# Optimization experiments

Hardware: AMD Instinct MI355X
Metric: run time of the kernel (lower is better)

## Reference

```python
import jax, jax.numpy as jnp
import numpy as np

N_NODES = 50000
N_EDGES = 800000
NODE_DIM = 128
IN_CH = 64
OUT_CH = 16
N_GRAPHS = 512
N_LAYERS = 5
BN_EPS = 1e-5


def setup_inputs() -> dict:
    key = jax.random.key(0)
    ks = jax.random.split(key, 16)
    s = lambda fan_in: 1.0 / np.sqrt(fan_in)
    inp = {
        "x": jax.random.normal(ks[0], (N_NODES, NODE_DIM), dtype=jnp.float32),
        "edge_index": jax.random.randint(ks[1], (2, N_EDGES), 0, N_NODES, dtype=jnp.int64),
        "batch": jnp.sort(jax.random.randint(ks[2], (N_NODES,), 0, N_GRAPHS, dtype=jnp.int64)),
        "enc_W": jax.random.normal(ks[3], (NODE_DIM, IN_CH), dtype=jnp.float32) * s(NODE_DIM),
        "enc_b": jnp.zeros((IN_CH,), dtype=jnp.float32),
        "conv_W1": jax.random.normal(ks[4], (N_LAYERS, IN_CH, IN_CH), dtype=jnp.float32) * s(IN_CH),
        "conv_b1": jnp.zeros((N_LAYERS, IN_CH), dtype=jnp.float32),
        "conv_W2": jax.random.normal(ks[5], (N_LAYERS, IN_CH, IN_CH), dtype=jnp.float32) * s(IN_CH),
        "conv_b2": jnp.zeros((N_LAYERS, IN_CH), dtype=jnp.float32),
        "bn_gamma": jnp.ones((N_LAYERS, IN_CH), dtype=jnp.float32),
        "bn_beta": jnp.zeros((N_LAYERS, IN_CH), dtype=jnp.float32),
        "fc1_W": jax.random.normal(ks[6], (IN_CH, IN_CH), dtype=jnp.float32) * s(IN_CH),
        "fc1_b": jnp.zeros((IN_CH,), dtype=jnp.float32),
        "fc2_W": jax.random.normal(ks[7], (IN_CH, OUT_CH), dtype=jnp.float32) * s(IN_CH),
        "fc2_b": jnp.zeros((OUT_CH,), dtype=jnp.float32),
    }
    return inp


def reference(x, edge_index, batch, enc_W, enc_b, conv_W1, conv_b1, conv_W2,
              conv_b2, bn_gamma, bn_beta, fc1_W, fc1_b, fc2_W, fc2_b):
    src, dst = edge_index[0], edge_index[1]
    # node feature encoder
    h = x @ enc_W + enc_b  # [N, C]
    for l in range(N_LAYERS):
        # GINConv (eps=0): (1+eps)*x + sum_{j->i} x_j, then 2-layer MLP
        agg = jax.ops.segment_sum(h[src], dst, num_segments=N_NODES)
        z = h + agg
        z = jax.nn.relu(z @ conv_W1[l] + conv_b1[l]) @ conv_W2[l] + conv_b2[l]
        z = jax.nn.relu(z)
        # BatchNorm1d (training stats, biased variance)
        mean = jnp.mean(z, axis=0)
        var = jnp.mean(jnp.square(z - mean), axis=0)
        h = (z - mean) * jax.lax.rsqrt(var + BN_EPS) * bn_gamma[l] + bn_beta[l]
    # global add pool over graphs
    g = jax.ops.segment_sum(h, batch, num_segments=N_GRAPHS)  # [G, C]
    g = jax.nn.relu(g @ fc1_W + fc1_b)
    # dropout is identity in eval mode
    out = g @ fc2_W + fc2_b  # [G, OUT_CH]
    return out
```

## Files before the change

kernel.cpp:

```cpp
#include <hip/hip_runtime.h>
#include <hip/hip_fp16.h>

#define N_NODES 50000
#define N_EDGES 800000
#define NODE_DIM 128
#define C 64
#define N_GRAPHS 512
#define N_LAYERS 5
#define BN_EPS 1e-5f

#define SCAN_BLOCKS 196
#define NBUCK 196
#define ECHUNK 4096

typedef unsigned int u32;
typedef unsigned short u16;

__device__ inline float2 h2f(u32 v) {
    __half2 h; __builtin_memcpy(&h, &v, 4);
    return __half22float2(h);
}
__device__ inline u32 f2h2(float a, float b) {
    __half2 h = __floats2half2_rn(a, b);
    u32 v; __builtin_memcpy(&v, &h, 4);
    return v;
}

__global__ __launch_bounds__(256) void enc_kernel(const float* __restrict__ x,
                                                  const float* __restrict__ W,
                                                  const float* __restrict__ b,
                                                  u32* __restrict__ z) {
    __shared__ float As[64 * 132];
    __shared__ float Ws[NODE_DIM * C];
    int t = threadIdx.x;
    int tc = t & 15, tr = t >> 4;
    for (int i = t; i < NODE_DIM * C; i += 256) Ws[i] = W[i];
    int row0 = blockIdx.x * 128;
    float4 bv = ((const float4*)b)[tc];
    float acc[8][4];
#pragma unroll
    for (int i = 0; i < 8; ++i) { acc[i][0] = bv.x; acc[i][1] = bv.y; acc[i][2] = bv.z; acc[i][3] = bv.w; }

    for (int kc = 0; kc < 2; ++kc) {
        __syncthreads();
        for (int it = 0; it < 8; ++it) {
            int idx = t + 256 * it;
            int r = idx >> 4, f4 = idx & 15;
            int grow = row0 + r;
            float4 v = (grow < N_NODES) ? ((const float4*)x)[grow * 32 + kc * 16 + f4]
                                        : make_float4(0.f, 0.f, 0.f, 0.f);
            int k4 = f4 * 4;
            As[(k4 + 0) * 132 + r] = v.x;
            As[(k4 + 1) * 132 + r] = v.y;
            As[(k4 + 2) * 132 + r] = v.z;
            As[(k4 + 3) * 132 + r] = v.w;
        }
        __syncthreads();
#pragma unroll 4
        for (int k = 0; k < 64; ++k) {
            const float* ap = As + k * 132 + tr * 8;
            float4 a0 = *(const float4*)(ap);
            float4 a1 = *(const float4*)(ap + 4);
            float4 w = *(const float4*)(Ws + (kc * 64 + k) * C + tc * 4);
            float av[8] = {a0.x, a0.y, a0.z, a0.w, a1.x, a1.y, a1.z, a1.w};
#pragma unroll
            for (int i = 0; i < 8; ++i) {
                acc[i][0] = fmaf(av[i], w.x, acc[i][0]);
                acc[i][1] = fmaf(av[i], w.y, acc[i][1]);
                acc[i][2] = fmaf(av[i], w.z, acc[i][2]);
                acc[i][3] = fmaf(av[i], w.w, acc[i][3]);
            }
        }
    }
#pragma unroll
    for (int i = 0; i < 8; ++i) {
        int grow = row0 + tr * 8 + i;
        if (grow < N_NODES) {
            uint2 o;
            o.x = f2h2(acc[i][0], acc[i][1]);
            o.y = f2h2(acc[i][2], acc[i][3]);
            ((uint2*)z)[grow * 16 + tc] = o;
        }
    }
}

__global__ __launch_bounds__(256) void csr_hist(const int* __restrict__ ei,
                                                int* __restrict__ bcount) {
    __shared__ int lhist[NBUCK];
    int t = threadIdx.x;
    if (t < NBUCK) lhist[t] = 0;
    __syncthreads();
    int e0 = blockIdx.x * ECHUNK;
    int e1 = min(e0 + ECHUNK, N_EDGES);
    for (int e = e0 + t; e < e1; e += 256)
        atomicAdd(&lhist[ei[N_EDGES + e] >> 8], 1);
    __syncthreads();
    if (t < NBUCK && lhist[t] > 0) atomicAdd(&bcount[t], lhist[t]);
}

__global__ __launch_bounds__(256) void csr_bscan(const int* __restrict__ bcount,
                                                 int* __restrict__ bbase,
                                                 int* __restrict__ bcursor,
                                                 int* __restrict__ offs) {
    __shared__ int s[256];
    int t = threadIdx.x;
    int v = (t < NBUCK) ? bcount[t] : 0;
    s[t] = v;
    for (int off = 1; off < 256; off <<= 1) {
        __syncthreads();
        int x = (t >= off) ? s[t - off] : 0;
        __syncthreads();
        s[t] += x;
    }
    __syncthreads();
    if (t < NBUCK) {
        bbase[t + 1] = s[t];
        bcursor[t] = s[t] - v;
    }
    if (t == 0) { bbase[0] = 0; offs[N_NODES] = N_EDGES; }
}

__global__ __launch_bounds__(256) void csr_stage(const int* __restrict__ ei,
                                                 int* __restrict__ bcursor,
                                                 u32* __restrict__ staged) {
    __shared__ int lhist[NBUCK];
    __shared__ int lbase[NBUCK];
    __shared__ int lcur[NBUCK];
    int t = threadIdx.x;
    if (t < NBUCK) lhist[t] = 0;
    __syncthreads();
    int e0 = blockIdx.x * ECHUNK;
    int e1 = min(e0 + ECHUNK, N_EDGES);
    for (int e = e0 + t; e < e1; e += 256)
        atomicAdd(&lhist[ei[N_EDGES + e] >> 8], 1);
    __syncthreads();
    if (t < NBUCK) {
        int c = lhist[t];
        lbase[t] = (c > 0) ? atomicAdd(&bcursor[t], c) : 0;
        lcur[t] = 0;
    }
    __syncthreads();
    for (int e = e0 + t; e < e1; e += 256) {
        int src = ei[e];
        int dst = ei[N_EDGES + e];
        int bk = dst >> 8;
        int r = atomicAdd(&lcur[bk], 1);
        staged[lbase[bk] + r] = (u32)src | ((u32)(dst & 255) << 16);
    }
}

__global__ __launch_bounds__(256) void csr_finalize(const u32* __restrict__ staged,
                                                    const int* __restrict__ bbase,
                                                    u16* __restrict__ csr,
                                                    int* __restrict__ offs) {
    __shared__ int lhist[256];
    __shared__ int lexc[256];
    __shared__ int lcur[256];
    int t = threadIdx.x;
    int b = blockIdx.x;
    int sbeg = bbase[b], send = bbase[b + 1];
    lhist[t] = 0;
    __syncthreads();
    for (int i = sbeg + t; i < send; i += 256)
        atomicAdd(&lhist[(staged[i] >> 16) & 255], 1);
    __syncthreads();
    int v = lhist[t];
    lexc[t] = v;
    for (int off = 1; off < 256; off <<= 1) {
        __syncthreads();
        int x = (t >= off) ? lexc[t - off] : 0;
        __syncthreads();
        lexc[t] += x;
    }
    __syncthreads();
    int excl = lexc[t] - v;
    int node = b * 256 + t;
    if (node < N_NODES) offs[node] = sbeg + excl;
    lcur[t] = excl;
    __syncthreads();
    for (int i = sbeg + t; i < send; i += 256) {
        u32 ent = staged[i];
        int dlow = (ent >> 16) & 255;
        int r = atomicAdd(&lcur[dlow], 1);
        csr[sbeg + r] = (u16)(ent & 0xFFFFu);
    }
}

__global__ __launch_bounds__(256) void gstart_kernel(const int* __restrict__ batch,
                                                     int* __restrict__ goffs) {
    int n = blockIdx.x * 256 + threadIdx.x;
    if (n >= N_NODES) return;
    if (n == 0) {
        for (int g = 0; g <= batch[0]; ++g) goffs[g] = 0;
    } else {
        int bp = batch[n - 1], bc = batch[n];
        for (int g = bp + 1; g <= bc; ++g) goffs[g] = n;
    }
    if (n == N_NODES - 1) {
        for (int g = batch[n] + 1; g <= N_GRAPHS; ++g) goffs[g] = N_NODES;
    }
}

__global__ __launch_bounds__(256, 8) void gather_kernel(const u16* __restrict__ csr_src,
                                                        const int* __restrict__ offs,
                                                        const u32* __restrict__ z_in,
                                                        const float* __restrict__ ss,
                                                        int use_ss,
                                                        u32* __restrict__ y) {
    int t = threadIdx.x;
    int tg = t & 7;
    int node = blockIdx.x * 32 + (t >> 3);
    if (node >= N_NODES) return;
    float scv[8], shv[8];
    if (use_ss) {
        float4 s0 = ((const float4*)ss)[tg * 2], s1 = ((const float4*)ss)[tg * 2 + 1];
        float4 h0 = ((const float4*)(ss + C))[tg * 2], h1 = ((const float4*)(ss + C))[tg * 2 + 1];
        scv[0] = s0.x; scv[1] = s0.y; scv[2] = s0.z; scv[3] = s0.w;
        scv[4] = s1.x; scv[5] = s1.y; scv[6] = s1.z; scv[7] = s1.w;
        shv[0] = h0.x; shv[1] = h0.y; shv[2] = h0.z; shv[3] = h0.w;
        shv[4] = h1.x; shv[5] = h1.y; shv[6] = h1.z; shv[7] = h1.w;
    } else {
#pragma unroll
        for (int i = 0; i < 8; ++i) { scv[i] = 1.f; shv[i] = 0.f; }
    }
    const uint4* z4 = (const uint4*)z_in;
    float acc[8];
    {
        uint4 sv = z4[node * 8 + tg];
        float2 p0 = h2f(sv.x), p1 = h2f(sv.y), p2 = h2f(sv.z), p3 = h2f(sv.w);
        acc[0] = p0.x; acc[1] = p0.y; acc[2] = p1.x; acc[3] = p1.y;
        acc[4] = p2.x; acc[5] = p2.y; acc[6] = p3.x; acc[7] = p3.y;
    }
    int beg = offs[node], end = offs[node + 1];
    int e = beg;
    for (; e + 3 < end; e += 4) {
        int s0 = csr_src[e], s1 = csr_src[e + 1], s2 = csr_src[e + 2], s3 = csr_src[e + 3];
        uint4 v0 = z4[s0 * 8 + tg], v1 = z4[s1 * 8 + tg];
        uint4 v2 = z4[s2 * 8 + tg], v3 = z4[s3 * 8 + tg];
        float2 a0 = h2f(v0.x), a1 = h2f(v1.x), a2 = h2f(v2.x), a3 = h2f(v3.x);
        acc[0] += (a0.x + a1.x) + (a2.x + a3.x);
        acc[1] += (a0.y + a1.y) + (a2.y + a3.y);
        a0 = h2f(v0.y); a1 = h2f(v1.y); a2 = h2f(v2.y); a3 = h2f(v3.y);
        acc[2] += (a0.x + a1.x) + (a2.x + a3.x);
        acc[3] += (a0.y + a1.y) + (a2.y + a3.y);
        a0 = h2f(v0.z); a1 = h2f(v1.z); a2 = h2f(v2.z); a3 = h2f(v3.z);
        acc[4] += (a0.x + a1.x) + (a2.x + a3.x);
        acc[5] += (a0.y + a1.y) + (a2.y + a3.y);
        a0 = h2f(v0.w); a1 = h2f(v1.w); a2 = h2f(v2.w); a3 = h2f(v3.w);
        acc[6] += (a0.x + a1.x) + (a2.x + a3.x);
        acc[7] += (a0.y + a1.y) + (a2.y + a3.y);
    }
    for (; e < end; ++e) {
        uint4 v = z4[csr_src[e] * 8 + tg];
        float2 a0 = h2f(v.x), a1 = h2f(v.y), a2 = h2f(v.z), a3 = h2f(v.w);
        acc[0] += a0.x; acc[1] += a0.y; acc[2] += a1.x; acc[3] += a1.y;
        acc[4] += a2.x; acc[5] += a2.y; acc[6] += a3.x; acc[7] += a3.y;
    }
    float cnt = (float)(end - beg + 1);
#pragma unroll
    for (int i = 0; i < 8; ++i) acc[i] = fmaf(acc[i], scv[i], cnt * shv[i]);
    uint4 o;
    o.x = f2h2(acc[0], acc[1]);
    o.y = f2h2(acc[2], acc[3]);
    o.z = f2h2(acc[4], acc[5]);
    o.w = f2h2(acc[6], acc[7]);
    ((uint4*)y)[node * 8 + tg] = o;
}

__global__ __launch_bounds__(256) void mlp_kernel(const u32* __restrict__ y,
                                                  u32* __restrict__ z_out,
                                                  const float* __restrict__ W1,
                                                  const float* __restrict__ b1,
                                                  const float* __restrict__ W2,
                                                  const float* __restrict__ b2,
                                                  float* __restrict__ stats) {
    __shared__ u32 Asw[32 * 68];
    __shared__ float Ws[C * C];
    int t = threadIdx.x;
    int tc = t & 15, tr = t >> 4;
    for (int i = t; i < C * C; i += 256) Ws[i] = W1[i];
    int row0 = blockIdx.x * 64;

    int tg = t & 7, rg = t >> 3;
    const uint4* y4 = (const uint4*)y;
#pragma unroll
    for (int it = 0; it < 2; ++it) {
        int r = rg + 32 * it;
        int node = row0 + r;
        uint4 v = (node < N_NODES) ? y4[node * 8 + tg] : make_uint4(0u, 0u, 0u, 0u);
        Asw[(tg * 4 + 0) * 68 + r] = v.x;
        Asw[(tg * 4 + 1) * 68 + r] = v.y;
        Asw[(tg * 4 + 2) * 68 + r] = v.z;
        Asw[(tg * 4 + 3) * 68 + r] = v.w;
    }
    __syncthreads();

    float4 b1v = ((const float4*)b1)[tc];
    float a[4][4];
#pragma unroll
    for (int i = 0; i < 4; ++i) { a[i][0] = b1v.x; a[i][1] = b1v.y; a[i][2] = b1v.z; a[i][3] = b1v.w; }
#pragma unroll 2
    for (int w = 0; w < 32; ++w) {
        uint4 aw = *(const uint4*)(Asw + w * 68 + tr * 4);
        float2 r0 = h2f(aw.x), r1 = h2f(aw.y), r2 = h2f(aw.z), r3 = h2f(aw.w);
        float4 w0 = *(const float4*)(Ws + (2 * w) * C + tc * 4);
        float4 w1 = *(const float4*)(Ws + (2 * w + 1) * C + tc * 4);
        float e0[4] = {r0.x, r1.x, r2.x, r3.x};
        float e1[4] = {r0.y, r1.y, r2.y, r3.y};
#pragma unroll
        for (int i = 0; i < 4; ++i) {
            a[i][0] = fmaf(e0[i], w0.x, a[i][0]); a[i][0] = fmaf(e1[i], w1.x, a[i][0]);
            a[i][1] = fmaf(e0[i], w0.y, a[i][1]); a[i][1] = fmaf(e1[i], w1.y, a[i][1]);
            a[i][2] = fmaf(e0[i], w0.z, a[i][2]); a[i][2] = fmaf(e1[i], w1.z, a[i][2]);
            a[i][3] = fmaf(e0[i], w0.w, a[i][3]); a[i][3] = fmaf(e1[i], w1.w, a[i][3]);
        }
    }
    __syncthreads();

    {
        uint4 w0, w1;
        w0.x = f2h2(fmaxf(a[0][0], 0.f), fmaxf(a[0][1], 0.f));
        w0.y = f2h2(fmaxf(a[1][0], 0.f), fmaxf(a[1][1], 0.f));
        w0.z = f2h2(fmaxf(a[2][0], 0.f), fmaxf(a[2][1], 0.f));
        w0.w = f2h2(fmaxf(a[3][0], 0.f), fmaxf(a[3][1], 0.f));
        w1.x = f2h2(fmaxf(a[0][2], 0.f), fmaxf(a[0][3], 0.f));
        w1.y = f2h2(fmaxf(a[1][2], 0.f), fmaxf(a[1][3], 0.f));
        w1.z = f2h2(fmaxf(a[2][2], 0.f), fmaxf(a[2][3], 0.f));
        w1.w = f2h2(fmaxf(a[3][2], 0.f), fmaxf(a[3][3], 0.f));
        *(uint4*)(Asw + (tc * 2) * 68 + tr * 4) = w0;
        *(uint4*)(Asw + (tc * 2 + 1) * 68 + tr * 4) = w1;
    }
    for (int i = t; i < C * C; i += 256) Ws[i] = W2[i];
    __syncthreads();

    float4 b2v = ((const float4*)b2)[tc];
#pragma unroll
    for (int i = 0; i < 4; ++i) { a[i][0] = b2v.x; a[i][1] = b2v.y; a[i][2] = b2v.z; a[i][3] = b2v.w; }
#pragma unroll 2
    for (int w = 0; w < 32; ++w) {
        uint4 aw = *(const uint4*)(Asw + w * 68 + tr * 4);
        float2 r0 = h2f(aw.x), r1 = h2f(aw.y), r2 = h2f(aw.z), r3 = h2f(aw.w);
        float4 w0 = *(const float4*)(Ws + (2 * w) * C + tc * 4);
        float4 w1 = *(const float4*)(Ws + (2 * w + 1) * C + tc * 4);
        float e0[4] = {r0.x, r1.x, r2.x, r3.x};
        float e1[4] = {r0.y, r1.y, r2.y, r3.y};
#pragma unroll
        for (int i = 0; i < 4; ++i) {
            a[i][0] = fmaf(e0[i], w0.x, a[i][0]); a[i][0] = fmaf(e1[i], w1.x, a[i][0]);
            a[i][1] = fmaf(e0[i], w0.y, a[i][1]); a[i][1] = fmaf(e1[i], w1.y, a[i][1]);
            a[i][2] = fmaf(e0[i], w0.z, a[i][2]); a[i][2] = fmaf(e1[i], w1.z, a[i][2]);
            a[i][3] = fmaf(e0[i], w0.w, a[i][3]); a[i][3] = fmaf(e1[i], w1.w, a[i][3]);
        }
    }

    float lsum[4] = {0.f, 0.f, 0.f, 0.f};
    float lsq[4] = {0.f, 0.f, 0.f, 0.f};
#pragma unroll
    for (int i = 0; i < 4; ++i) {
        int grow = row0 + tr * 4 + i;
        if (grow < N_NODES) {
            float o0 = fmaxf(a[i][0], 0.f), o1 = fmaxf(a[i][1], 0.f);
            float o2 = fmaxf(a[i][2], 0.f), o3 = fmaxf(a[i][3], 0.f);
            uint2 o;
            o.x = f2h2(o0, o1);
            o.y = f2h2(o2, o3);
            ((uint2*)z_out)[grow * 16 + tc] = o;
            lsum[0] += o0; lsum[1] += o1; lsum[2] += o2; lsum[3] += o3;
            lsq[0] += o0 * o0; lsq[1] += o1 * o1; lsq[2] += o2 * o2; lsq[3] += o3 * o3;
        }
    }
    __syncthreads();
    float* red = Ws;
#pragma unroll
    for (int j = 0; j < 4; ++j) {
        red[tr * 128 + tc * 4 + j] = lsum[j];
        red[tr * 128 + 64 + tc * 4 + j] = lsq[j];
    }
    __syncthreads();
    if (t < 128) {
        float s = 0.f;
#pragma unroll
        for (int r = 0; r < 16; ++r) s += red[r * 128 + t];
        atomicAdd(&stats[t], s);
    }
}

__global__ void bn_finalize(const float* __restrict__ stats,
                            const float* __restrict__ gamma,
                            const float* __restrict__ beta,
                            float* __restrict__ ss) {
    int c = threadIdx.x;
    if (c >= C) return;
    const float invN = 1.0f / (float)N_NODES;
    float mean = stats[c] * invN;
    float var = stats[C + c] * invN - mean * mean;
    float rstd = rsqrtf(var + BN_EPS);
    float sc = gamma[c] * rstd;
    ss[c] = sc;
    ss[C + c] = beta[c] - mean * sc;
}

__global__ __launch_bounds__(256) void pool_kernel(const u32* __restrict__ z,
                                                   const float* __restrict__ ss,
                                                   const int* __restrict__ goffs,
                                                   float* __restrict__ g) {
    __shared__ float4 red[256];
    int t = threadIdx.x;
    int tc = t & 15, tr = t >> 4;
    int gr = blockIdx.x;
    int beg = goffs[gr], end = goffs[gr + 1];
    const uint2* z2 = (const uint2*)z;
    float4 acc = make_float4(0.f, 0.f, 0.f, 0.f);
    for (int n = beg + tr; n < end; n += 16) {
        uint2 v = z2[n * 16 + tc];
        float2 a = h2f(v.x), c = h2f(v.y);
        acc.x += a.x; acc.y += a.y; acc.z += c.x; acc.w += c.y;
    }
    red[tr * 16 + tc] = acc;
    for (int s = 8; s > 0; s >>= 1) {
        __syncthreads();
        if (tr < s) {
            float4 o = red[(tr + s) * 16 + tc];
            float4 m = red[tr * 16 + tc];
            m.x += o.x; m.y += o.y; m.z += o.z; m.w += o.w;
            red[tr * 16 + tc] = m;
        }
    }
    __syncthreads();
    if (tr == 0) {
        float4 sum = red[tc];
        float4 sc = ((const float4*)ss)[tc];
        float4 sh = ((const float4*)(ss + C))[tc];
        float cnt = (float)(end - beg);
        float4 o;
        o.x = fmaf(sum.x, sc.x, cnt * sh.x);
        o.y = fmaf(sum.y, sc.y, cnt * sh.y);
        o.z = fmaf(sum.z, sc.z, cnt * sh.z);
        o.w = fmaf(sum.w, sc.w, cnt * sh.w);
        ((float4*)g)[gr * 16 + tc] = o;
    }
}

__global__ __launch_bounds__(256) void head_kernel(const float* __restrict__ g,
                                                   const float* __restrict__ fc1W,
                                                   const float* __restrict__ fc1b,
                                                   const float* __restrict__ fc2W,
                                                   const float* __restrict__ fc2b,
                                                   float* __restrict__ out) {
    __shared__ float W1s[C * C];
    __shared__ float W2s[C * 16];
    __shared__ float gs[4][C], t1s[4][C];
    int t = threadIdx.x;
    for (int i = t; i < C * C; i += 256) W1s[i] = fc1W[i];
    for (int i = t; i < C * 16; i += 256) W2s[i] = fc2W[i];
    int ch = t & 63, rr = t >> 6;
    int g0 = blockIdx.x * 4;
    gs[rr][ch] = g[(g0 + rr) * C + ch];
    __syncthreads();
    float a1 = fc1b[ch];
#pragma unroll 8
    for (int k = 0; k < C; ++k) a1 = fmaf(gs[rr][k], W1s[k * C + ch], a1);
    t1s[rr][ch] = fmaxf(a1, 0.f);
    __syncthreads();
    if (t < 64) {
        int o = t & 15, r2 = t >> 4;
        float a2 = fc2b[o];
#pragma unroll 8
        for (int k = 0; k < C; ++k) a2 = fmaf(t1s[r2][k], W2s[k * 16 + o], a2);
        out[(g0 + r2) * 16 + o] = a2;
    }
}

extern "C" void kernel_launch(void* const* d_in, const int* in_sizes, int n_in,
                              void* d_out, int out_size, void* d_ws, size_t ws_size,
                              hipStream_t stream) {
    const float* x    = (const float*)d_in[0];
    const int*   ei   = (const int*)d_in[1];
    const int*   batch= (const int*)d_in[2];
    const float* encW = (const float*)d_in[3];
    const float* encb = (const float*)d_in[4];
    const float* cW1  = (const float*)d_in[5];
    const float* cb1  = (const float*)d_in[6];
    const float* cW2  = (const float*)d_in[7];
    const float* cb2  = (const float*)d_in[8];
    const float* gam  = (const float*)d_in[9];
    const float* bet  = (const float*)d_in[10];
    const float* f1W  = (const float*)d_in[11];
    const float* f1b  = (const float*)d_in[12];
    const float* f2W  = (const float*)d_in[13];
    const float* f2b  = (const float*)d_in[14];
    float* out = (float*)d_out;

    char* ws = (char*)d_ws;
    u32*   zA      = (u32*)  (ws);
    u32*   zB      = (u32*)  (ws + 6400000);
    u32*   ybuf    = (u32*)  (ws + 12800000);
    u16*   csr     = (u16*)  (ws + 19200000);
    u32*   staged  = (u32*)  (ws + 20800000);
    int*   offs    = (int*)  (ws + 24000000);
    int*   bcount  = (int*)  (ws + 24200064);
    int*   bbase   = (int*)  (ws + 24201088);
    int*   bcursor = (int*)  (ws + 24202112);
    float* stats   = (float*)(ws + 24203136);
    float* ssb     = (float*)(ws + 24205696);
    int*   goffs   = (int*)  (ws + 24208256);
    float* gpool   = (float*)(ws + 24210432);

    hipMemsetAsync(bcount, 0, NBUCK * sizeof(int), stream);
    hipMemsetAsync(stats, 0, 5 * 2 * C * sizeof(float), stream);
    csr_hist<<<NBUCK, 256, 0, stream>>>(ei, bcount);
    csr_bscan<<<1, 256, 0, stream>>>(bcount, bbase, bcursor, offs);
    csr_stage<<<NBUCK, 256, 0, stream>>>(ei, bcursor, staged);
    csr_finalize<<<NBUCK, 256, 0, stream>>>(staged, bbase, csr, offs);
    gstart_kernel<<<SCAN_BLOCKS, 256, 0, stream>>>(batch, goffs);

    enc_kernel<<<(N_NODES + 127) / 128, 256, 0, stream>>>(x, encW, encb, zA);

    u32* zin = zA;
    u32* zout = zB;
    for (int l = 0; l < N_LAYERS; ++l) {
        const float* ss_prev = (l > 0) ? (ssb + (size_t)(l - 1) * 2 * C) : ssb;
        gather_kernel<<<(N_NODES * 8 + 255) / 256, 256, 0, stream>>>(
            csr, offs, zin, ss_prev, l > 0 ? 1 : 0, ybuf);
        mlp_kernel<<<(N_NODES + 63) / 64, 256, 0, stream>>>(
            ybuf, zout,
            cW1 + (size_t)l * C * C, cb1 + (size_t)l * C,
            cW2 + (size_t)l * C * C, cb2 + (size_t)l * C,
            stats + (size_t)l * 2 * C);
        bn_finalize<<<1, 64, 0, stream>>>(stats + (size_t)l * 2 * C,
                                          gam + (size_t)l * C, bet + (size_t)l * C,
                                          ssb + (size_t)l * 2 * C);
        u32* tmp = zin; zin = zout; zout = tmp;
    }

    pool_kernel<<<N_GRAPHS, 256, 0, stream>>>(zin, ssb + (size_t)(N_LAYERS - 1) * 2 * C, goffs, gpool);
    head_kernel<<<N_GRAPHS / 4, 256, 0, stream>>>(gpool, f1W, f1b, f2W, f2b, out);
}
```

Measured before the change: 424.4 us.

## Split node features into two channel planes and gather each plane separately

Node feature storage becomes two planes of 32 half channels each (PLANE offset), so each gather pass touches a 3.2MB working set that fits better in cache. The gather is launched twice per layer, one pass per plane, with 4 threads per node instead of 8. The encoder, MLP and pool kernels are updated to read and write the planar layout. The gather output uses nontemporal stores. The trade-off is that the CSR indices are read twice per layer and there is an extra launch.

```diff
diff --git a/kernel.cpp b/kernel.cpp
--- a/kernel.cpp
+++ b/kernel.cpp
@@ -12,9 +12,11 @@
 #define SCAN_BLOCKS 196
 #define NBUCK 196
 #define ECHUNK 4096
+#define PLANE 800000
 
 typedef unsigned int u32;
 typedef unsigned short u16;
+typedef u32 u32x4 __attribute__((ext_vector_type(4)));
 
 __device__ inline float2 h2f(u32 v) {
     __half2 h; __builtin_memcpy(&h, &v, 4);
@@ -72,6 +74,7 @@
             }
         }
     }
+    u32* zp = z + (tc >> 3) * PLANE;
 #pragma unroll
     for (int i = 0; i < 8; ++i) {
         int grow = row0 + tr * 8 + i;
@@ -79,7 +82,7 @@
             uint2 o;
             o.x = f2h2(acc[i][0], acc[i][1]);
             o.y = f2h2(acc[i][2], acc[i][3]);
-            ((uint2*)z)[grow * 16 + tc] = o;
+            ((uint2*)zp)[grow * 8 + (tc & 7)] = o;
         }
     }
 }
@@ -201,20 +204,22 @@
     }
 }
 
-__global__ __launch_bounds__(256, 8) void gather_kernel(const u16* __restrict__ csr_src,
-                                                        const int* __restrict__ offs,
-                                                        const u32* __restrict__ z_in,
-                                                        const float* __restrict__ ss,
-                                                        int use_ss,
-                                                        u32* __restrict__ y) {
-    int t = threadIdx.x;
-    int tg = t & 7;
-    int node = blockIdx.x * 32 + (t >> 3);
+__global__ __launch_bounds__(256, 8) void gather_plane_kernel(const u16* __restrict__ csr_src,
+                                                              const int* __restrict__ offs,
+                                                              const u32* __restrict__ z_base,
+                                                              int plane,
+                                                              const float* __restrict__ ss,
+                                                              int use_ss,
+                                                              u32* __restrict__ y_base) {
+    int t = threadIdx.x;
+    int tg = t & 3;
+    int node = blockIdx.x * 64 + (t >> 2);
     if (node >= N_NODES) return;
     float scv[8], shv[8];
     if (use_ss) {
-        float4 s0 = ((const float4*)ss)[tg * 2], s1 = ((const float4*)ss)[tg * 2 + 1];
-        float4 h0 = ((const float4*)(ss + C))[tg * 2], h1 = ((const float4*)(ss + C))[tg * 2 + 1];
+        int f4i = plane * 8 + tg * 2;
+        float4 s0 = ((const float4*)ss)[f4i], s1 = ((const float4*)ss)[f4i + 1];
+        float4 h0 = ((const float4*)(ss + C))[f4i], h1 = ((const float4*)(ss + C))[f4i + 1];
         scv[0] = s0.x; scv[1] = s0.y; scv[2] = s0.z; scv[3] = s0.w;
         scv[4] = s1.x; scv[5] = s1.y; scv[6] = s1.z; scv[7] = s1.w;
         shv[0] = h0.x; shv[1] = h0.y; shv[2] = h0.z; shv[3] = h0.w;
@@ -223,10 +228,10 @@
 #pragma unroll
         for (int i = 0; i < 8; ++i) { scv[i] = 1.f; shv[i] = 0.f; }
     }
-    const uint4* z4 = (const uint4*)z_in;
+    const uint4* zp = (const uint4*)(z_base + plane * PLANE);
     float acc[8];
     {
-        uint4 sv = z4[node * 8 + tg];
+        uint4 sv = zp[node * 4 + tg];
         float2 p0 = h2f(sv.x), p1 = h2f(sv.y), p2 = h2f(sv.z), p3 = h2f(sv.w);
         acc[0] = p0.x; acc[1] = p0.y; acc[2] = p1.x; acc[3] = p1.y;
         acc[4] = p2.x; acc[5] = p2.y; acc[6] = p3.x; acc[7] = p3.y;
@@ -235,8 +240,8 @@
     int e = beg;
     for (; e + 3 < end; e += 4) {
         int s0 = csr_src[e], s1 = csr_src[e + 1], s2 = csr_src[e + 2], s3 = csr_src[e + 3];
-        uint4 v0 = z4[s0 * 8 + tg], v1 = z4[s1 * 8 + tg];
-        uint4 v2 = z4[s2 * 8 + tg], v3 = z4[s3 * 8 + tg];
+        uint4 v0 = zp[s0 * 4 + tg], v1 = zp[s1 * 4 + tg];
+        uint4 v2 = zp[s2 * 4 + tg], v3 = zp[s3 * 4 + tg];
         float2 a0 = h2f(v0.x), a1 = h2f(v1.x), a2 = h2f(v2.x), a3 = h2f(v3.x);
         acc[0] += (a0.x + a1.x) + (a2.x + a3.x);
         acc[1] += (a0.y + a1.y) + (a2.y + a3.y);
@@ -251,7 +256,7 @@
         acc[7] += (a0.y + a1.y) + (a2.y + a3.y);
     }
     for (; e < end; ++e) {
-        uint4 v = z4[csr_src[e] * 8 + tg];
+        uint4 v = zp[csr_src[e] * 4 + tg];
         float2 a0 = h2f(v.x), a1 = h2f(v.y), a2 = h2f(v.z), a3 = h2f(v.w);
         acc[0] += a0.x; acc[1] += a0.y; acc[2] += a1.x; acc[3] += a1.y;
         acc[4] += a2.x; acc[5] += a2.y; acc[6] += a3.x; acc[7] += a3.y;
@@ -259,12 +264,13 @@
     float cnt = (float)(end - beg + 1);
 #pragma unroll
     for (int i = 0; i < 8; ++i) acc[i] = fmaf(acc[i], scv[i], cnt * shv[i]);
-    uint4 o;
+    u32x4 o;
     o.x = f2h2(acc[0], acc[1]);
     o.y = f2h2(acc[2], acc[3]);
     o.z = f2h2(acc[4], acc[5]);
     o.w = f2h2(acc[6], acc[7]);
-    ((uint4*)y)[node * 8 + tg] = o;
+    u32x4* yp = (u32x4*)(y_base + plane * PLANE);
+    __builtin_nontemporal_store(o, &yp[node * 4 + tg]);
 }
 
 __global__ __launch_bounds__(256) void mlp_kernel(const u32* __restrict__ y,
@@ -282,12 +288,13 @@
     int row0 = blockIdx.x * 64;
 
     int tg = t & 7, rg = t >> 3;
-    const uint4* y4 = (const uint4*)y;
+    const uint4* yp = (const uint4*)(y + (tg >> 2) * PLANE);
+    int q = tg & 3;
 #pragma unroll
     for (int it = 0; it < 2; ++it) {
         int r = rg + 32 * it;
         int node = row0 + r;
-        uint4 v = (node < N_NODES) ? y4[node * 8 + tg] : make_uint4(0u, 0u, 0u, 0u);
+        uint4 v = (node < N_NODES) ? yp[node * 4 + q] : make_uint4(0u, 0u, 0u, 0u);
         Asw[(tg * 4 + 0) * 68 + r] = v.x;
         Asw[(tg * 4 + 1) * 68 + r] = v.y;
         Asw[(tg * 4 + 2) * 68 + r] = v.z;
@@ -355,6 +362,7 @@
 
     float lsum[4] = {0.f, 0.f, 0.f, 0.f};
     float lsq[4] = {0.f, 0.f, 0.f, 0.f};
+    u32* zo = z_out + (tc >> 3) * PLANE;
 #pragma unroll
     for (int i = 0; i < 4; ++i) {
         int grow = row0 + tr * 4 + i;
@@ -364,7 +372,7 @@
             uint2 o;
             o.x = f2h2(o0, o1);
             o.y = f2h2(o2, o3);
-            ((uint2*)z_out)[grow * 16 + tc] = o;
+            ((uint2*)zo)[grow * 8 + (tc & 7)] = o;
             lsum[0] += o0; lsum[1] += o1; lsum[2] += o2; lsum[3] += o3;
             lsq[0] += o0 * o0; lsq[1] += o1 * o1; lsq[2] += o2 * o2; lsq[3] += o3 * o3;
         }
@@ -409,10 +417,11 @@
     int tc = t & 15, tr = t >> 4;
     int gr = blockIdx.x;
     int beg = goffs[gr], end = goffs[gr + 1];
-    const uint2* z2 = (const uint2*)z;
+    const uint2* zp = (const uint2*)(z + (tc >> 3) * PLANE);
+    int w = tc & 7;
     float4 acc = make_float4(0.f, 0.f, 0.f, 0.f);
     for (int n = beg + tr; n < end; n += 16) {
-        uint2 v = z2[n * 16 + tc];
+        uint2 v = zp[n * 8 + w];
         float2 a = h2f(v.x), c = h2f(v.y);
         acc.x += a.x; acc.y += a.y; acc.z += c.x; acc.w += c.y;
     }
@@ -520,8 +529,10 @@
     u32* zout = zB;
     for (int l = 0; l < N_LAYERS; ++l) {
         const float* ss_prev = (l > 0) ? (ssb + (size_t)(l - 1) * 2 * C) : ssb;
-        gather_kernel<<<(N_NODES * 8 + 255) / 256, 256, 0, stream>>>(
-            csr, offs, zin, ss_prev, l > 0 ? 1 : 0, ybuf);
+        gather_plane_kernel<<<(N_NODES + 63) / 64, 256, 0, stream>>>(
+            csr, offs, zin, 0, ss_prev, l > 0 ? 1 : 0, ybuf);
+        gather_plane_kernel<<<(N_NODES + 63) / 64, 256, 0, stream>>>(
+            csr, offs, zin, 1, ss_prev, l > 0 ? 1 : 0, ybuf);
         mlp_kernel<<<(N_NODES + 63) / 64, 256, 0, stream>>>(
             ybuf, zout,
             cW1 + (size_t)l * C * C, cb1 + (size_t)l * C,
```

Measured after the change: 465.3 us. 9.6% more time.
